# Optimization experiments

Hardware: AMD Instinct MI355X
Metric: run time of the kernel (lower is better)

The kernel has to match this reference:

```python
import jax, jax.numpy as jnp
import numpy as np

B, S, HID = 2, 2048, 2048
NH = 16
Q_LORA, KV_LORA = 1024, 512
NOPE, ROPE, VD = 128, 64, 128
QK = NOPE + ROPE  # 192
EPS = 1e-6
THETA = 10000.0


def rms_norm(x, w, eps=EPS):
    x32 = x.astype(jnp.float32)
    var = jnp.mean(x32 * x32, axis=-1, keepdims=True)
    return (w * (x32 * jax.lax.rsqrt(var + eps))).astype(x.dtype)


def rotate_half(x):
    h = x.shape[-1] // 2
    return jnp.concatenate([-x[..., h:], x[..., :h]], axis=-1)


def setup_inputs() -> dict:
    key = jax.random.key(0)
    ks = jax.random.split(key, 8)
    hidden_states = jax.random.normal(ks[0], (B, S, HID), dtype=jnp.float32)
    attention_mask = jnp.zeros((B, 1, 1, S), dtype=jnp.float32)
    # RoPE tables (true rotary values)
    inv_freq = 1.0 / (THETA ** (np.arange(0, ROPE, 2, dtype=np.float32) / ROPE))
    pos = np.arange(S, dtype=np.float32)
    freqs = np.outer(pos, inv_freq)  # [S, ROPE/2]
    emb = np.concatenate([freqs, freqs], axis=-1)  # [S, ROPE]
    cos = jnp.asarray(np.cos(emb), dtype=jnp.float32)
    sin = jnp.asarray(np.sin(emb), dtype=jnp.float32)
    # Parameters, stored as [in, out] so y = x @ W
    sd = lambda fan_in: 1.0 / np.sqrt(fan_in)
    w_q_down = jax.random.normal(ks[1], (HID, Q_LORA), dtype=jnp.float32) * sd(HID)
    w_q_up = jax.random.normal(ks[2], (Q_LORA, NH * QK), dtype=jnp.float32) * sd(Q_LORA)
    w_kv_down = jax.random.normal(ks[3], (HID, KV_LORA + ROPE), dtype=jnp.float32) * sd(HID)
    w_kv_up = jax.random.normal(ks[4], (KV_LORA, NH * (NOPE + VD)), dtype=jnp.float32) * sd(KV_LORA)
    w_o = jax.random.normal(ks[5], (NH * VD, HID), dtype=jnp.float32) * sd(NH * VD)
    q_norm_w = jnp.ones((Q_LORA,), dtype=jnp.float32)
    kv_norm_w = jnp.ones((KV_LORA,), dtype=jnp.float32)
    return dict(hidden_states=hidden_states, attention_mask=attention_mask,
                cos=cos, sin=sin, w_q_down=w_q_down, w_q_up=w_q_up,
                w_kv_down=w_kv_down, w_kv_up=w_kv_up, w_o=w_o,
                q_norm_w=q_norm_w, kv_norm_w=kv_norm_w)


def reference(hidden_states, attention_mask, cos, sin,
              w_q_down, w_q_up, w_kv_down, w_kv_up, w_o,
              q_norm_w, kv_norm_w):
    b, s, _ = hidden_states.shape
    # --- Q path: down-proj -> RMSNorm -> up-proj ---
    q = rms_norm(hidden_states @ w_q_down, q_norm_w) @ w_q_up  # [b,s,NH*QK]
    q = q.reshape(b, s, NH, QK).transpose(0, 2, 1, 3)          # [b,h,s,QK]
    q_nope, q_rope = q[..., :NOPE], q[..., NOPE:]
    # --- KV path: down-proj -> split latent / rope key -> up-proj ---
    kv = hidden_states @ w_kv_down                              # [b,s,KV_LORA+ROPE]
    kv_latent, k_rope = kv[..., :KV_LORA], kv[..., KV_LORA:]
    kv_up = rms_norm(kv_latent, kv_norm_w) @ w_kv_up            # [b,s,NH*(NOPE+VD)]
    kv_up = kv_up.reshape(b, s, NH, NOPE + VD).transpose(0, 2, 1, 3)
    k_nope, v = kv_up[..., :NOPE], kv_up[..., NOPE:]            # [b,h,s,*]
    k_rope = k_rope[:, None, :, :]                              # [b,1,s,ROPE] (broadcast over heads)
    # --- partial RoPE ---
    c = cos[None, None, :, :]
    sn = sin[None, None, :, :]
    q_rope = q_rope * c + rotate_half(q_rope) * sn
    k_rope = k_rope * c + rotate_half(k_rope) * sn
    q_final = jnp.concatenate([q_nope, q_rope], axis=-1)        # [b,h,s,QK]
    k_final = jnp.concatenate([k_nope, jnp.broadcast_to(k_rope, (b, NH, s, ROPE))], axis=-1)
    # --- SDPA (non-causal, additive mask) ---
    scale = 1.0 / jnp.sqrt(jnp.asarray(QK, dtype=jnp.float32))
    scores = jnp.einsum('bhqd,bhkd->bhqk', q_final, k_final) * scale
    scores = scores + attention_mask                            # [b,1,1,s] broadcast
    probs = jax.nn.softmax(scores.astype(jnp.float32), axis=-1).astype(q_final.dtype)
    attn = jnp.einsum('bhqk,bhkd->bhqd', probs, v)              # [b,h,s,VD]
    attn = attn.transpose(0, 2, 1, 3).reshape(b, s, NH * VD)
    return attn @ w_o
```

## Files before the change

### kernel.cpp

```cpp
#include <hip/hip_runtime.h>
#include <hip/hip_bf16.h>

typedef unsigned short u16;
typedef unsigned int u32;
typedef short s16x8 __attribute__((ext_vector_type(8)));
typedef float f32x4 __attribute__((ext_vector_type(4)));
typedef float f32x2 __attribute__((ext_vector_type(2)));

__device__ __forceinline__ float bf2f(u16 u) {
    union { u32 i; float f; } v; v.i = ((u32)u) << 16; return v.f;
}
__device__ __forceinline__ u16 f2bf(float f) {
    union { float f; u32 i; } v; v.f = f;
    u32 i = v.i;
    u32 r = (i + 0x7FFFu + ((i >> 16) & 1u)) >> 16;
    return (u16)r;
}

__device__ __forceinline__ void gl2lds16(const u16* g, u16* l) {
    __builtin_amdgcn_global_load_lds(
        (const __attribute__((address_space(1))) u32*)g,
        (__attribute__((address_space(3))) u32*)l, 16, 0, 0);
}

__global__ __launch_bounds__(256) void cvt_f32_bf16(
    const float* __restrict__ in, u16* __restrict__ out, long long n2)
{
    long long i = (long long)blockIdx.x * 256 + threadIdx.x;
    if (i < n2) {
        f32x2 v = *(const f32x2*)(in + i * 2);
        u32 p = (u32)f2bf(v[0]) | ((u32)f2bf(v[1]) << 16);
        *(u32*)(out + i * 2) = p;
    }
}

__global__ __launch_bounds__(256) void transpose_f32_bf16(
    const float* __restrict__ in, u16* __restrict__ out, int R, int C)
{
    __shared__ u16 t[32][33];
    int tx = threadIdx.x & 31, ty = threadIdx.x >> 5;
    int c0 = blockIdx.x * 32, r0 = blockIdx.y * 32;
    #pragma unroll
    for (int i = 0; i < 32; i += 8)
        t[ty + i][tx] = f2bf(in[(size_t)(r0 + ty + i) * C + c0 + tx]);
    __syncthreads();
    #pragma unroll
    for (int i = 0; i < 32; i += 8)
        out[(size_t)(c0 + ty + i) * R + r0 + tx] = t[tx][ty + i];
}

__global__ __launch_bounds__(256) void transpose_v(
    const u16* __restrict__ kvup, u16* __restrict__ vt)
{
    __shared__ u16 t[32][33];
    int tx = threadIdx.x & 31, ty = threadIdx.x >> 5;
    int s0 = blockIdx.x * 32, v0 = blockIdx.y * 32;
    int b = blockIdx.z >> 4, h = blockIdx.z & 15;
    #pragma unroll
    for (int i = 0; i < 32; i += 8)
        t[ty + i][tx] = kvup[(size_t)(b * 2048 + s0 + ty + i) * 4096 + h * 256 + 128 + v0 + tx];
    __syncthreads();
    #pragma unroll
    for (int i = 0; i < 32; i += 8)
        vt[((size_t)(b * 16 + h) * 128 + v0 + ty + i) * 2048 + s0 + tx] = t[tx][ty + i];
}

__global__ __launch_bounds__(256) void gemm_bf16(
    const u16* __restrict__ A, const u16* __restrict__ Bt, u16* __restrict__ C,
    int M, int N, int K)
{
    __shared__ u16 As[64][40];
    __shared__ u16 Bs[64][40];

    const int tid  = threadIdx.x;
    const int wave = tid >> 6, lane = tid & 63;
    const int quad = lane >> 4, l16 = lane & 15;
    const int m0 = blockIdx.y * 64, n0 = blockIdx.x * 64;
    const int wm = (wave >> 1) * 32, wn = (wave & 1) * 32;

    const int srow = tid >> 2;
    const int koff = (tid & 3) * 8;

    f32x4 acc00 = {0.f,0.f,0.f,0.f};
    f32x4 acc01 = {0.f,0.f,0.f,0.f};
    f32x4 acc10 = {0.f,0.f,0.f,0.f};
    f32x4 acc11 = {0.f,0.f,0.f,0.f};

    for (int k0 = 0; k0 < K; k0 += 32) {
        *(s16x8*)&As[srow][koff] = *(const s16x8*)&A[(size_t)(m0 + srow) * K + k0 + koff];
        *(s16x8*)&Bs[srow][koff] = *(const s16x8*)&Bt[(size_t)(n0 + srow) * K + k0 + koff];
        __syncthreads();
        s16x8 a0 = *(const s16x8*)&As[wm + l16][quad * 8];
        s16x8 a1 = *(const s16x8*)&As[wm + 16 + l16][quad * 8];
        s16x8 b0 = *(const s16x8*)&Bs[wn + l16][quad * 8];
        s16x8 b1 = *(const s16x8*)&Bs[wn + 16 + l16][quad * 8];
        acc00 = __builtin_amdgcn_mfma_f32_16x16x32_bf16(a0, b0, acc00, 0, 0, 0);
        acc01 = __builtin_amdgcn_mfma_f32_16x16x32_bf16(a0, b1, acc01, 0, 0, 0);
        acc10 = __builtin_amdgcn_mfma_f32_16x16x32_bf16(a1, b0, acc10, 0, 0, 0);
        acc11 = __builtin_amdgcn_mfma_f32_16x16x32_bf16(a1, b1, acc11, 0, 0, 0);
        __syncthreads();
    }

    #pragma unroll
    for (int r = 0; r < 4; ++r) {
        int row0 = m0 + wm + quad * 4 + r;
        int col0 = n0 + wn + l16;
        C[(size_t)row0 * N + col0]             = f2bf(acc00[r]);
        C[(size_t)row0 * N + col0 + 16]        = f2bf(acc01[r]);
        C[(size_t)(row0 + 16) * N + col0]      = f2bf(acc10[r]);
        C[(size_t)(row0 + 16) * N + col0 + 16] = f2bf(acc11[r]);
    }
}

template <typename OUT>
__global__ __launch_bounds__(256) void gemm128(
    const u16* __restrict__ A, const u16* __restrict__ Bt, OUT* __restrict__ C,
    int M, int N, int K)
{
    __shared__ u16 As[128 * 32];
    __shared__ u16 Bs[128 * 32];

    const int tid  = threadIdx.x;
    const int wave = tid >> 6, lane = tid & 63;
    const int quad = lane >> 4, l16 = lane & 15;
    const int m0 = blockIdx.y * 128, n0 = blockIdx.x * 128;
    const int wm = (wave >> 1) * 64, wn = (wave & 1) * 64;

    const int srow = lane >> 2, soct = (lane & 3) * 8;

    f32x4 acc[4][4];
    #pragma unroll
    for (int i = 0; i < 4; ++i)
        #pragma unroll
        for (int j = 0; j < 4; ++j) acc[i][j] = (f32x4){0.f,0.f,0.f,0.f};

    for (int k0 = 0; k0 < K; k0 += 32) {
        #pragma unroll
        for (int op = 0; op < 2; ++op) {
            int g = wave * 2 + op;
            gl2lds16(&A[(size_t)(m0 + g * 16 + srow) * K + k0 + soct], &As[g * 512]);
            gl2lds16(&Bt[(size_t)(n0 + g * 16 + srow) * K + k0 + soct], &Bs[g * 512]);
        }
        __syncthreads();
        s16x8 af[4], bf[4];
        #pragma unroll
        for (int i = 0; i < 4; ++i) {
            af[i] = *(const s16x8*)&As[(wm + i * 16 + l16) * 32 + quad * 8];
            bf[i] = *(const s16x8*)&Bs[(wn + i * 16 + l16) * 32 + quad * 8];
        }
        #pragma unroll
        for (int i = 0; i < 4; ++i)
            #pragma unroll
            for (int j = 0; j < 4; ++j)
                acc[i][j] = __builtin_amdgcn_mfma_f32_16x16x32_bf16(af[i], bf[j], acc[i][j], 0, 0, 0);
        __syncthreads();
    }

    #pragma unroll
    for (int i = 0; i < 4; ++i) {
        #pragma unroll
        for (int j = 0; j < 4; ++j) {
            #pragma unroll
            for (int r = 0; r < 4; ++r) {
                int row = m0 + wm + i * 16 + quad * 4 + r;
                int col = n0 + wn + j * 16 + l16;
                if constexpr (sizeof(OUT) == 2)
                    C[(size_t)row * N + col] = f2bf(acc[i][j][r]);
                else
                    C[(size_t)row * N + col] = acc[i][j][r];
            }
        }
    }
}

__global__ __launch_bounds__(256) void rmsnorm_kernel(
    const u16* __restrict__ in, const float* __restrict__ w, u16* __restrict__ out,
    int len, int istride, int ostride)
{
    const int row = blockIdx.x, tid = threadIdx.x;
    const u16* x = in + (size_t)row * istride;
    float ss = 0.f;
    for (int i = tid; i < len; i += 256) { float v = bf2f(x[i]); ss += v * v; }
    #pragma unroll
    for (int off = 32; off >= 1; off >>= 1) ss += __shfl_xor(ss, off, 64);
    __shared__ float wsum[4];
    if ((tid & 63) == 0) wsum[tid >> 6] = ss;
    __syncthreads();
    float tot = wsum[0] + wsum[1] + wsum[2] + wsum[3];
    float inv = 1.0f / sqrtf(tot / (float)len + 1e-6f);
    for (int i = tid; i < len; i += 256) {
        float v = bf2f(x[i]);
        out[(size_t)row * ostride + i] = f2bf(v * inv * w[i]);
    }
}

__global__ __launch_bounds__(256) void rope_kernel(
    u16* __restrict__ qb, const u16* __restrict__ kvb, u16* __restrict__ krot,
    const float* __restrict__ cosb, const float* __restrict__ sinb)
{
    const int row = blockIdx.x;
    const int s = row & 2047;
    const int lane = threadIdx.x & 63, wave = threadIdx.x >> 6;
    const float c  = cosb[s * 64 + lane];
    const float sn = sinb[s * 64 + lane];
    for (int seg = wave; seg < 17; seg += 4) {
        const u16* pin; u16* pout;
        if (seg < 16) { pout = qb + (size_t)row * 3072 + seg * 192 + 128; pin = pout; }
        else          { pin = kvb + (size_t)row * 576 + 512; pout = krot + (size_t)row * 64; }
        float x  = bf2f(pin[lane]);
        float xp = bf2f(pin[lane ^ 32]);
        float rot = (lane < 32) ? -xp : xp;
        pout[lane] = f2bf(x * c + rot * sn);
    }
}

__global__ __launch_bounds__(256, 2) void attn_mfma4(
    const u16* __restrict__ qb,
    const u16* __restrict__ kvup,
    const u16* __restrict__ krot,
    const u16* __restrict__ vt,
    const float* __restrict__ mask,
    u16* __restrict__ attnb)
{
    __shared__ u16 Ks[64 * 200];
    __shared__ u16 Ps[128 * 72];
    __shared__ u16 Vd[2][128 * 64];

    const int tid  = threadIdx.x;
    const int wave = tid >> 6, lane = tid & 63;
    const int quad = lane >> 4, l16 = lane & 15;
    const int qt = blockIdx.x, h = blockIdx.y, b = blockIdx.z;
    const int row0 = b * 2048 + qt * 128;
    const int qw = wave * 16;
    const float scale2 = 0.10411610f;
    const float l2e    = 1.4426950408889634f;
    const int swz = (l16 & 7) << 3;

    s16x8 onesf;
    #pragma unroll
    for (int j = 0; j < 8; ++j) onesf[j] = (short)0x3F80;

    s16x8 qf[2][6];
    #pragma unroll
    for (int s = 0; s < 2; ++s)
        #pragma unroll
        for (int kc = 0; kc < 6; ++kc)
            qf[s][kc] = *(const s16x8*)&qb[(size_t)(row0 + s * 64 + qw + l16) * 3072
                                           + h * 192 + kc * 32 + quad * 8];

    const u16* pk[6]; int offk[6], stepk[6];
    #pragma unroll
    for (int i = 0; i < 6; ++i) {
        int idx = tid + i * 256;
        int r = idx / 24, c = (idx % 24) * 8;
        offk[i] = r * 200 + c;
        if (c < 128) { pk[i] = kvup + (size_t)(b * 2048 + r) * 4096 + h * 256 + c; stepk[i] = 64 * 4096; }
        else         { pk[i] = krot + (size_t)(b * 2048 + r) * 64 + (c - 128);     stepk[i] = 64 * 64;   }
    }

    const u16* vtb = vt + (size_t)(b * 16 + h) * 128 * 2048;
    const u16* pv[4];
    #pragma unroll
    for (int i = 0; i < 4; ++i) {
        int widx = i * 4 + wave;
        int r = widx * 8 + (lane >> 3);
        int u = (lane & 7) ^ (lane >> 3);
        pv[i] = vtb + (size_t)r * 2048 + u * 8;
    }

    s16x8 kreg[6];
    #pragma unroll
    for (int i = 0; i < 6; ++i) { kreg[i] = *(const s16x8*)pk[i]; pk[i] += stepk[i]; }
    #pragma unroll
    for (int i = 0; i < 4; ++i) {
        gl2lds16(pv[i], &Vd[0][(i * 4 + wave) * 512]);
        pv[i] += 64;
    }

    float m = -__builtin_inff();
    f32x4 l[2] = {(f32x4){0.f,0.f,0.f,0.f}, (f32x4){0.f,0.f,0.f,0.f}};
    f32x4 O[2][8];
    #pragma unroll
    for (int s = 0; s < 2; ++s)
        #pragma unroll
        for (int vi = 0; vi < 8; ++vi) O[s][vi] = (f32x4){0.f,0.f,0.f,0.f};

    for (int kt = 0; kt < 32; ++kt) {
        __syncthreads();
        #pragma unroll
        for (int i = 0; i < 6; ++i) *(s16x8*)&Ks[offk[i]] = kreg[i];
        __syncthreads();

        if (kt < 31) {
            #pragma unroll
            for (int i = 0; i < 6; ++i) { kreg[i] = *(const s16x8*)pk[i]; pk[i] += stepk[i]; }
            #pragma unroll
            for (int i = 0; i < 4; ++i) {
                gl2lds16(pv[i], &Vd[(kt + 1) & 1][(i * 4 + wave) * 512]);
                pv[i] += 64;
            }
        }
        float mv4[4];
        #pragma unroll
        for (int ct = 0; ct < 4; ++ct)
            mv4[ct] = mask[b * 2048 + kt * 64 + ct * 16 + l16] * l2e;

        f32x4 S[2][4];
        #pragma unroll
        for (int s = 0; s < 2; ++s)
            #pragma unroll
            for (int ct = 0; ct < 4; ++ct) S[s][ct] = (f32x4){0.f,0.f,0.f,0.f};
        __builtin_amdgcn_s_setprio(1);
        #pragma unroll
        for (int kc = 0; kc < 6; ++kc) {
            #pragma unroll
            for (int ct = 0; ct < 4; ++ct) {
                s16x8 bfr = *(const s16x8*)&Ks[(ct * 16 + l16) * 200 + kc * 32 + quad * 8];
                S[0][ct] = __builtin_amdgcn_mfma_f32_16x16x32_bf16(qf[0][kc], bfr, S[0][ct], 0, 0, 0);
                S[1][ct] = __builtin_amdgcn_mfma_f32_16x16x32_bf16(qf[1][kc], bfr, S[1][ct], 0, 0, 0);
            }
        }
        __builtin_amdgcn_s_setprio(0);

        #pragma unroll
        for (int ct = 0; ct < 4; ++ct)
            #pragma unroll
            for (int s = 0; s < 2; ++s)
                #pragma unroll
                for (int r = 0; r < 4; ++r) S[s][ct][r] = S[s][ct][r] * scale2 + mv4[ct];

        float tm = S[0][0][0];
        #pragma unroll
        for (int s = 0; s < 2; ++s)
            #pragma unroll
            for (int ct = 0; ct < 4; ++ct)
                #pragma unroll
                for (int r = 0; r < 4; ++r) tm = fmaxf(tm, S[s][ct][r]);
        #pragma unroll
        for (int off = 1; off < 64; off <<= 1)
            tm = fmaxf(tm, __shfl_xor(tm, off, 64));
        float mn = fmaxf(m, tm);
        float alpha = exp2f(m - mn);
        m = mn;

        #pragma unroll
        for (int s = 0; s < 2; ++s)
            #pragma unroll
            for (int ct = 0; ct < 4; ++ct)
                #pragma unroll
                for (int r = 0; r < 4; ++r)
                    Ps[(s * 64 + qw + quad * 4 + r) * 72 + ct * 16 + l16]
                        = f2bf(exp2f(S[s][ct][r] - m));

        #pragma unroll
        for (int s = 0; s < 2; ++s) {
            l[s] *= alpha;
            #pragma unroll
            for (int vi = 0; vi < 8; ++vi) O[s][vi] *= alpha;
        }

        const u16* Vb = Vd[kt & 1];
        __builtin_amdgcn_s_setprio(1);
        #pragma unroll
        for (int kc = 0; kc < 2; ++kc) {
            s16x8 a0 = *(const s16x8*)&Ps[(qw + l16) * 72 + kc * 32 + quad * 8];
            s16x8 a1 = *(const s16x8*)&Ps[(64 + qw + l16) * 72 + kc * 32 + quad * 8];
            #pragma unroll
            for (int vi = 0; vi < 8; ++vi) {
                int rowv = vi * 16 + l16;
                int col  = kc * 32 + quad * 8;
                s16x8 bfr = *(const s16x8*)&Vb[rowv * 64 + (col ^ swz)];
                O[0][vi] = __builtin_amdgcn_mfma_f32_16x16x32_bf16(a0, bfr, O[0][vi], 0, 0, 0);
                O[1][vi] = __builtin_amdgcn_mfma_f32_16x16x32_bf16(a1, bfr, O[1][vi], 0, 0, 0);
            }
            l[0] = __builtin_amdgcn_mfma_f32_16x16x32_bf16(a0, onesf, l[0], 0, 0, 0);
            l[1] = __builtin_amdgcn_mfma_f32_16x16x32_bf16(a1, onesf, l[1], 0, 0, 0);
        }
        __builtin_amdgcn_s_setprio(0);
    }

    #pragma unroll
    for (int s = 0; s < 2; ++s) {
        f32x4 linv;
        #pragma unroll
        for (int r = 0; r < 4; ++r) linv[r] = 1.0f / l[s][r];
        #pragma unroll
        for (int vi = 0; vi < 8; ++vi) {
            #pragma unroll
            for (int r = 0; r < 4; ++r) {
                int q_ = row0 + s * 64 + qw + quad * 4 + r;
                attnb[(size_t)q_ * 2048 + h * 128 + vi * 16 + l16] = f2bf(O[s][vi][r] * linv[r]);
            }
        }
    }
}

extern "C" void kernel_launch(void* const* d_in, const int* in_sizes, int n_in,
                              void* d_out, int out_size, void* d_ws, size_t ws_size,
                              hipStream_t stream)
{
    const float* hidden = (const float*)d_in[0];
    const float* mask   = (const float*)d_in[1];
    const float* cosb   = (const float*)d_in[2];
    const float* sinb   = (const float*)d_in[3];
    const float* w_qd   = (const float*)d_in[4];
    const float* w_qu   = (const float*)d_in[5];
    const float* w_kvd  = (const float*)d_in[6];
    const float* w_kvu  = (const float*)d_in[7];
    const float* w_o    = (const float*)d_in[8];
    const float* qnw    = (const float*)d_in[9];
    const float* kvnw   = (const float*)d_in[10];
    float* out = (float*)d_out;

    u16* ws = (u16*)d_ws;
    u16* qbuf   = ws + 0;
    u16* wt_qd  = ws + 0;
    u16* kvup   = ws + 12582912;
    u16* hid_bf = ws + 12582912;
    u16* wt_kvd = ws + 20971520;
    u16* attnb  = ws + 29360128;
    u16* qd     = ws + 29360128;
    u16* wt_qu  = ws + 33554432;
    u16* kvb    = ws + 37748736;
    u16* wt_o   = ws + 37748736;
    u16* kvn    = ws + 40108032;
    u16* wt_kvu = ws + 42205184;
    u16* krot   = ws + 44302336;
    u16* vt     = ws + 44564480;

    {
        long long n2 = (long long)4096 * 2048 / 2;
        cvt_f32_bf16<<<(int)((n2 + 255) / 256), 256, 0, stream>>>(hidden, hid_bf, n2);
    }

    transpose_f32_bf16<<<dim3(32, 64), 256, 0, stream>>>(w_qd, wt_qd, 2048, 1024);
    gemm128<u16><<<dim3(8, 32), 256, 0, stream>>>(hid_bf, wt_qd, qd, 4096, 1024, 2048);
    rmsnorm_kernel<<<4096, 256, 0, stream>>>(qd, qnw, qd, 1024, 1024, 1024);
    transpose_f32_bf16<<<dim3(96, 32), 256, 0, stream>>>(w_qu, wt_qu, 1024, 3072);
    gemm128<u16><<<dim3(24, 32), 256, 0, stream>>>(qd, wt_qu, qbuf, 4096, 3072, 1024);

    transpose_f32_bf16<<<dim3(18, 64), 256, 0, stream>>>(w_kvd, wt_kvd, 2048, 576);
    gemm_bf16<<<dim3(9, 64), 256, 0, stream>>>(hid_bf, wt_kvd, kvb, 4096, 576, 2048);
    rmsnorm_kernel<<<4096, 256, 0, stream>>>(kvb, kvnw, kvn, 512, 576, 512);
    transpose_f32_bf16<<<dim3(128, 16), 256, 0, stream>>>(w_kvu, wt_kvu, 512, 4096);
    gemm128<u16><<<dim3(32, 32), 256, 0, stream>>>(kvn, wt_kvu, kvup, 4096, 4096, 512);

    transpose_v<<<dim3(64, 4, 32), 256, 0, stream>>>(kvup, vt);

    rope_kernel<<<4096, 256, 0, stream>>>(qbuf, kvb, krot, cosb, sinb);
    transpose_f32_bf16<<<dim3(64, 64), 256, 0, stream>>>(w_o, wt_o, 2048, 2048);

    attn_mfma4<<<dim3(16, 16, 2), 256, 0, stream>>>(qbuf, kvup, krot, vt, mask, attnb);

    gemm128<float><<<dim3(16, 32), 256, 0, stream>>>(attnb, wt_o, out, 4096, 2048, 2048);
}
```

Baseline: 515.2 us.

## Restructure attention to transposed 32x32 MFMA with register-resident probabilities

Rewrites the attention kernel to compute S^T = K·Q^T with 32x32x16 MFMAs, so each lane owns one query column. The softmax row max and sum then need only a single cross-half shuffle instead of a full-wave reduction. Probabilities are packed to bf16 with v_cvt_pk_bf16_f32 and rearranged by lane shuffles straight into PV MFMA operands, removing the Ps LDS round-trip and the ones-matrix MFMA used for row sums. The risks are higher register pressure from the f32x16 accumulators and a bespoke shuffle layout that has to line up exactly with the MFMA operand format.

```diff
diff --git a/kernel.cpp b/kernel.cpp
--- a/kernel.cpp
+++ b/kernel.cpp
@@ -6,6 +6,8 @@
 typedef short s16x8 __attribute__((ext_vector_type(8)));
 typedef float f32x4 __attribute__((ext_vector_type(4)));
 typedef float f32x2 __attribute__((ext_vector_type(2)));
+typedef float f32x16 __attribute__((ext_vector_type(16)));
+typedef u32 u32x2 __attribute__((ext_vector_type(2)));
 
 __device__ __forceinline__ float bf2f(u16 u) {
     union { u32 i; float f; } v; v.i = ((u32)u) << 16; return v.f;
@@ -15,6 +17,14 @@
     u32 i = v.i;
     u32 r = (i + 0x7FFFu + ((i >> 16) & 1u)) >> 16;
     return (u16)r;
+}
+__device__ __forceinline__ u32 cvtpk_bf16(float lo, float hi) {
+    u32 r;
+    asm("v_cvt_pk_bf16_f32 %0, %1, %2" : "=v"(r) : "v"(lo), "v"(hi));
+    return r;
+}
+__device__ __forceinline__ float bitf(u32 x) {
+    union { u32 i; float f; } v; v.i = x; return v.f;
 }
 
 __device__ __forceinline__ void gl2lds16(const u16* g, u16* l) {
@@ -214,7 +224,7 @@
     }
 }
 
-__global__ __launch_bounds__(256, 2) void attn_mfma4(
+__global__ __launch_bounds__(256, 2) void attn_mfma5(
     const u16* __restrict__ qb,
     const u16* __restrict__ kvup,
     const u16* __restrict__ krot,
@@ -223,39 +233,31 @@
     u16* __restrict__ attnb)
 {
     __shared__ u16 Ks[64 * 200];
-    __shared__ u16 Ps[128 * 72];
     __shared__ u16 Vd[2][128 * 64];
 
     const int tid  = threadIdx.x;
     const int wave = tid >> 6, lane = tid & 63;
-    const int quad = lane >> 4, l16 = lane & 15;
+    const int l31  = lane & 31;
+    const int hi   = lane >> 5;
     const int qt = blockIdx.x, h = blockIdx.y, b = blockIdx.z;
     const int row0 = b * 2048 + qt * 128;
-    const int qw = wave * 16;
+    const int qrow = row0 + wave * 32 + l31;
     const float scale2 = 0.10411610f;
     const float l2e    = 1.4426950408889634f;
-    const int swz = (l16 & 7) << 3;
-
-    s16x8 onesf;
-    #pragma unroll
-    for (int j = 0; j < 8; ++j) onesf[j] = (short)0x3F80;
-
-    s16x8 qf[2][6];
-    #pragma unroll
-    for (int s = 0; s < 2; ++s)
-        #pragma unroll
-        for (int kc = 0; kc < 6; ++kc)
-            qf[s][kc] = *(const s16x8*)&qb[(size_t)(row0 + s * 64 + qw + l16) * 3072
-                                           + h * 192 + kc * 32 + quad * 8];
-
-    const u16* pk[6]; int offk[6], stepk[6];
+
+    s16x8 qf[12];
+    #pragma unroll
+    for (int kc = 0; kc < 12; ++kc)
+        qf[kc] = *(const s16x8*)&qb[(size_t)qrow * 3072 + h * 192 + kc * 16 + hi * 8];
+
+    const u16* kp[6]; int offk[6], stepk[6];
     #pragma unroll
     for (int i = 0; i < 6; ++i) {
         int idx = tid + i * 256;
         int r = idx / 24, c = (idx % 24) * 8;
         offk[i] = r * 200 + c;
-        if (c < 128) { pk[i] = kvup + (size_t)(b * 2048 + r) * 4096 + h * 256 + c; stepk[i] = 64 * 4096; }
-        else         { pk[i] = krot + (size_t)(b * 2048 + r) * 64 + (c - 128);     stepk[i] = 64 * 64;   }
+        if (c < 128) { kp[i] = kvup + (size_t)(b * 2048 + r) * 4096 + h * 256 + c; stepk[i] = 64 * 4096; }
+        else         { kp[i] = krot + (size_t)(b * 2048 + r) * 64 + (c - 128);     stepk[i] = 64 * 64;   }
     }
 
     const u16* vtb = vt + (size_t)(b * 16 + h) * 128 * 2048;
@@ -270,20 +272,20 @@
 
     s16x8 kreg[6];
     #pragma unroll
-    for (int i = 0; i < 6; ++i) { kreg[i] = *(const s16x8*)pk[i]; pk[i] += stepk[i]; }
+    for (int i = 0; i < 6; ++i) { kreg[i] = *(const s16x8*)kp[i]; kp[i] += stepk[i]; }
     #pragma unroll
     for (int i = 0; i < 4; ++i) {
         gl2lds16(pv[i], &Vd[0][(i * 4 + wave) * 512]);
         pv[i] += 64;
     }
 
-    float m = -__builtin_inff();
-    f32x4 l[2] = {(f32x4){0.f,0.f,0.f,0.f}, (f32x4){0.f,0.f,0.f,0.f}};
-    f32x4 O[2][8];
-    #pragma unroll
-    for (int s = 0; s < 2; ++s)
-        #pragma unroll
-        for (int vi = 0; vi < 8; ++vi) O[s][vi] = (f32x4){0.f,0.f,0.f,0.f};
+    float m_run = -__builtin_inff();
+    float l_run = 0.f;
+    f32x16 O[4];
+    #pragma unroll
+    for (int v = 0; v < 4; ++v)
+        #pragma unroll
+        for (int e = 0; e < 16; ++e) O[v][e] = 0.f;
 
     for (int kt = 0; kt < 32; ++kt) {
         __syncthreads();
@@ -293,104 +295,125 @@
 
         if (kt < 31) {
             #pragma unroll
-            for (int i = 0; i < 6; ++i) { kreg[i] = *(const s16x8*)pk[i]; pk[i] += stepk[i]; }
+            for (int i = 0; i < 6; ++i) { kreg[i] = *(const s16x8*)kp[i]; kp[i] += stepk[i]; }
             #pragma unroll
             for (int i = 0; i < 4; ++i) {
                 gl2lds16(pv[i], &Vd[(kt + 1) & 1][(i * 4 + wave) * 512]);
                 pv[i] += 64;
             }
         }
-        float mv4[4];
-        #pragma unroll
-        for (int ct = 0; ct < 4; ++ct)
-            mv4[ct] = mask[b * 2048 + kt * 64 + ct * 16 + l16] * l2e;
-
-        f32x4 S[2][4];
-        #pragma unroll
-        for (int s = 0; s < 2; ++s)
-            #pragma unroll
-            for (int ct = 0; ct < 4; ++ct) S[s][ct] = (f32x4){0.f,0.f,0.f,0.f};
+
+        f32x16 St[2];
+        #pragma unroll
+        for (int t = 0; t < 2; ++t)
+            #pragma unroll
+            for (int e = 0; e < 16; ++e) St[t][e] = 0.f;
         __builtin_amdgcn_s_setprio(1);
         #pragma unroll
-        for (int kc = 0; kc < 6; ++kc) {
-            #pragma unroll
-            for (int ct = 0; ct < 4; ++ct) {
-                s16x8 bfr = *(const s16x8*)&Ks[(ct * 16 + l16) * 200 + kc * 32 + quad * 8];
-                S[0][ct] = __builtin_amdgcn_mfma_f32_16x16x32_bf16(qf[0][kc], bfr, S[0][ct], 0, 0, 0);
-                S[1][ct] = __builtin_amdgcn_mfma_f32_16x16x32_bf16(qf[1][kc], bfr, S[1][ct], 0, 0, 0);
+        for (int kc = 0; kc < 12; ++kc) {
+            s16x8 a0 = *(const s16x8*)&Ks[(l31)      * 200 + kc * 16 + hi * 8];
+            s16x8 a1 = *(const s16x8*)&Ks[(32 + l31) * 200 + kc * 16 + hi * 8];
+            St[0] = __builtin_amdgcn_mfma_f32_32x32x16_bf16(a0, qf[kc], St[0], 0, 0, 0);
+            St[1] = __builtin_amdgcn_mfma_f32_32x32x16_bf16(a1, qf[kc], St[1], 0, 0, 0);
+        }
+        __builtin_amdgcn_s_setprio(0);
+
+        #pragma unroll
+        for (int t = 0; t < 2; ++t)
+            #pragma unroll
+            for (int g = 0; g < 4; ++g) {
+                f32x4 mk = *(const f32x4*)&mask[b * 2048 + kt * 64 + t * 32 + g * 8 + hi * 4];
+                #pragma unroll
+                for (int e = 0; e < 4; ++e)
+                    St[t][g * 4 + e] = St[t][g * 4 + e] * scale2 + mk[e] * l2e;
             }
-        }
-        __builtin_amdgcn_s_setprio(0);
-
-        #pragma unroll
-        for (int ct = 0; ct < 4; ++ct)
-            #pragma unroll
-            for (int s = 0; s < 2; ++s)
+
+        float tm = St[0][0];
+        #pragma unroll
+        for (int t = 0; t < 2; ++t)
+            #pragma unroll
+            for (int e = 0; e < 16; ++e) tm = fmaxf(tm, St[t][e]);
+        tm = fmaxf(tm, __shfl_xor(tm, 32, 64));
+        float mn = fmaxf(m_run, tm);
+        float alpha = exp2f(m_run - mn);
+        m_run = mn;
+
+        u32 pkw[2][4][2];
+        #pragma unroll
+        for (int t = 0; t < 2; ++t)
+            #pragma unroll
+            for (int g = 0; g < 4; ++g) {
+                float e0 = exp2f(St[t][g * 4 + 0] - mn);
+                float e1 = exp2f(St[t][g * 4 + 1] - mn);
+                float e2 = exp2f(St[t][g * 4 + 2] - mn);
+                float e3 = exp2f(St[t][g * 4 + 3] - mn);
+                pkw[t][g][0] = cvtpk_bf16(e0, e1);
+                pkw[t][g][1] = cvtpk_bf16(e2, e3);
+            }
+
+        float rs = 0.f;
+        #pragma unroll
+        for (int t = 0; t < 2; ++t)
+            #pragma unroll
+            for (int g = 0; g < 4; ++g)
                 #pragma unroll
-                for (int r = 0; r < 4; ++r) S[s][ct][r] = S[s][ct][r] * scale2 + mv4[ct];
-
-        float tm = S[0][0][0];
-        #pragma unroll
-        for (int s = 0; s < 2; ++s)
-            #pragma unroll
-            for (int ct = 0; ct < 4; ++ct)
-                #pragma unroll
-                for (int r = 0; r < 4; ++r) tm = fmaxf(tm, S[s][ct][r]);
-        #pragma unroll
-        for (int off = 1; off < 64; off <<= 1)
-            tm = fmaxf(tm, __shfl_xor(tm, off, 64));
-        float mn = fmaxf(m, tm);
-        float alpha = exp2f(m - mn);
-        m = mn;
-
-        #pragma unroll
-        for (int s = 0; s < 2; ++s)
-            #pragma unroll
-            for (int ct = 0; ct < 4; ++ct)
-                #pragma unroll
-                for (int r = 0; r < 4; ++r)
-                    Ps[(s * 64 + qw + quad * 4 + r) * 72 + ct * 16 + l16]
-                        = f2bf(exp2f(S[s][ct][r] - m));
-
-        #pragma unroll
-        for (int s = 0; s < 2; ++s) {
-            l[s] *= alpha;
-            #pragma unroll
-            for (int vi = 0; vi < 8; ++vi) O[s][vi] *= alpha;
+                for (int p = 0; p < 2; ++p) {
+                    u32 w = pkw[t][g][p];
+                    rs += bitf(w << 16) + bitf(w & 0xFFFF0000u);
+                }
+        rs += __shfl_xor(rs, 32, 64);
+        l_run = l_run * alpha + rs;
+
+        #pragma unroll
+        for (int v = 0; v < 4; ++v)
+            #pragma unroll
+            for (int e = 0; e < 16; ++e) O[v][e] *= alpha;
+
+        s16x8 pb[4];
+        #pragma unroll
+        for (int c = 0; c < 4; ++c) {
+            const int t = c >> 1, cl = c & 1;
+            u32 snd0 = hi ? pkw[t][2 * cl][0] : pkw[t][2 * cl + 1][0];
+            u32 snd1 = hi ? pkw[t][2 * cl][1] : pkw[t][2 * cl + 1][1];
+            u32 rc0 = (u32)__shfl_xor((int)snd0, 32, 64);
+            u32 rc1 = (u32)__shfl_xor((int)snd1, 32, 64);
+            u32 w0 = hi ? rc0 : pkw[t][2 * cl][0];
+            u32 w1 = hi ? rc1 : pkw[t][2 * cl][1];
+            u32 w2 = hi ? pkw[t][2 * cl + 1][0] : rc0;
+            u32 w3 = hi ? pkw[t][2 * cl + 1][1] : rc1;
+            union { u32 w[4]; s16x8 v; } uu;
+            uu.w[0] = w0; uu.w[1] = w1; uu.w[2] = w2; uu.w[3] = w3;
+            pb[c] = uu.v;
         }
 
         const u16* Vb = Vd[kt & 1];
         __builtin_amdgcn_s_setprio(1);
         #pragma unroll
-        for (int kc = 0; kc < 2; ++kc) {
-            s16x8 a0 = *(const s16x8*)&Ps[(qw + l16) * 72 + kc * 32 + quad * 8];
-            s16x8 a1 = *(const s16x8*)&Ps[(64 + qw + l16) * 72 + kc * 32 + quad * 8];
-            #pragma unroll
-            for (int vi = 0; vi < 8; ++vi) {
-                int rowv = vi * 16 + l16;
-                int col  = kc * 32 + quad * 8;
-                s16x8 bfr = *(const s16x8*)&Vb[rowv * 64 + (col ^ swz)];
-                O[0][vi] = __builtin_amdgcn_mfma_f32_16x16x32_bf16(a0, bfr, O[0][vi], 0, 0, 0);
-                O[1][vi] = __builtin_amdgcn_mfma_f32_16x16x32_bf16(a1, bfr, O[1][vi], 0, 0, 0);
+        for (int c = 0; c < 4; ++c) {
+            #pragma unroll
+            for (int v = 0; v < 4; ++v) {
+                int rv = v * 32 + l31;
+                int unit = (c * 2 + hi) ^ (l31 & 7);
+                s16x8 af = *(const s16x8*)&Vb[rv * 64 + unit * 8];
+                O[v] = __builtin_amdgcn_mfma_f32_32x32x16_bf16(af, pb[c], O[v], 0, 0, 0);
             }
-            l[0] = __builtin_amdgcn_mfma_f32_16x16x32_bf16(a0, onesf, l[0], 0, 0, 0);
-            l[1] = __builtin_amdgcn_mfma_f32_16x16x32_bf16(a1, onesf, l[1], 0, 0, 0);
         }
         __builtin_amdgcn_s_setprio(0);
     }
 
-    #pragma unroll
-    for (int s = 0; s < 2; ++s) {
-        f32x4 linv;
-        #pragma unroll
-        for (int r = 0; r < 4; ++r) linv[r] = 1.0f / l[s][r];
-        #pragma unroll
-        for (int vi = 0; vi < 8; ++vi) {
-            #pragma unroll
-            for (int r = 0; r < 4; ++r) {
-                int q_ = row0 + s * 64 + qw + quad * 4 + r;
-                attnb[(size_t)q_ * 2048 + h * 128 + vi * 16 + l16] = f2bf(O[s][vi][r] * linv[r]);
-            }
+    float linv = 1.0f / l_run;
+    #pragma unroll
+    for (int v = 0; v < 4; ++v) {
+        #pragma unroll
+        for (int g = 0; g < 4; ++g) {
+            float o0 = O[v][g * 4 + 0] * linv;
+            float o1 = O[v][g * 4 + 1] * linv;
+            float o2 = O[v][g * 4 + 2] * linv;
+            float o3 = O[v][g * 4 + 3] * linv;
+            u32 w0 = (u32)f2bf(o0) | ((u32)f2bf(o1) << 16);
+            u32 w1 = (u32)f2bf(o2) | ((u32)f2bf(o3) << 16);
+            size_t off = (size_t)qrow * 2048 + h * 128 + v * 32 + g * 8 + hi * 4;
+            *(u32x2*)&attnb[off] = (u32x2){w0, w1};
         }
     }
 }
@@ -450,7 +473,7 @@
     rope_kernel<<<4096, 256, 0, stream>>>(qbuf, kvb, krot, cosb, sinb);
     transpose_f32_bf16<<<dim3(64, 64), 256, 0, stream>>>(w_o, wt_o, 2048, 2048);
 
-    attn_mfma4<<<dim3(16, 16, 2), 256, 0, stream>>>(qbuf, kvup, krot, vt, mask, attnb);
+    attn_mfma5<<<dim3(16, 16, 2), 256, 0, stream>>>(qbuf, kvup, krot, vt, mask, attnb);
 
     gemm128<float><<<dim3(16, 32), 256, 0, stream>>>(attnb, wt_o, out, 4096, 2048, 2048);
 }
```

Result: slower. 537.8 us (+4.4%).
